# Kernel tuning notes

Hardware: AMD Instinct MI355X
Metric: run time of the kernel (lower is better)

Reference implementation:

```python
import jax, jax.numpy as jnp
import numpy as np

B, T, D = 2, 2048, 1024
H = 16
HD = D // H  # 64
A = 16
MLP_H = 4 * D
EPS = 1e-6


def rmsnorm(x, w):
    # x: [..., C], w: [C]
    return x * jax.lax.rsqrt(jnp.mean(x * x, axis=-1, keepdims=True) + EPS) * w


def setup_inputs() -> dict:
    key = jax.random.key(0)
    ks = jax.random.split(key, 24)
    s = 0.02
    inp = {
        'x': jax.random.normal(ks[0], (B, T, D), jnp.float32),
        'actions': jax.random.normal(ks[1], (B, T, A), jnp.float32),
        # block norms
        'n1_w': jnp.ones((D,), jnp.float32),
        'n2_w': jnp.ones((D,), jnp.float32),
        # attention projections (stored [in, out])
        'q_w': jax.random.normal(ks[2], (D, D), jnp.float32) * s,
        'q_b': jnp.zeros((D,), jnp.float32),
        'k_w': jax.random.normal(ks[3], (D, D), jnp.float32) * s,
        'k_b': jnp.zeros((D,), jnp.float32),
        'v_w': jax.random.normal(ks[4], (D, D), jnp.float32) * s,
        'v_b': jnp.zeros((D,), jnp.float32),
        'qn_w': jnp.ones((HD,), jnp.float32),
        'kn_w': jnp.ones((HD,), jnp.float32),
        'o_w': jax.random.normal(ks[5], (D, D), jnp.float32) * s,
        'o_b': jnp.zeros((D,), jnp.float32),
        # action conditioning
        'ae1_w': jax.random.normal(ks[6], (A, D), jnp.float32) * s,
        'ae1_b': jnp.zeros((D,), jnp.float32),
        'ae2_w': jax.random.normal(ks[7], (D, D), jnp.float32) * s,
        'ae2_b': jnp.zeros((D,), jnp.float32),
        'mod_w': jax.random.normal(ks[8], (D, 4 * D), jnp.float32) * s,
        'mod_b': jnp.zeros((4 * D,), jnp.float32),
        # mlp
        'm1_w': jax.random.normal(ks[9], (D, MLP_H), jnp.float32) * s,
        'm1_b': jnp.zeros((MLP_H,), jnp.float32),
        'm2_w': jax.random.normal(ks[10], (MLP_H, D), jnp.float32) * s,
        'm2_b': jnp.zeros((D,), jnp.float32),
    }
    return inp


def _forward(x, actions, n1_w, n2_w, q_w, q_b, k_w, k_b, v_w, v_b, qn_w, kn_w,
             o_w, o_b, ae1_w, ae1_b, ae2_w, ae2_b, mod_w, mod_b,
             m1_w, m1_b, m2_w, m2_b):
    Bc, Tc, Dc = x.shape
    scale = HD ** -0.5

    # --- causal temporal attention with QK RMSNorm ---
    h = rmsnorm(x, n1_w)
    q = (h @ q_w + q_b).reshape(Bc, Tc, H, HD).transpose(0, 2, 1, 3)  # [B,H,T,hd]
    k = (h @ k_w + k_b).reshape(Bc, Tc, H, HD).transpose(0, 2, 1, 3)
    v = (h @ v_w + v_b).reshape(Bc, Tc, H, HD).transpose(0, 2, 1, 3)
    q = rmsnorm(q, qn_w)
    k = rmsnorm(k, kn_w)
    attn = jnp.einsum('bhqd,bhkd->bhqk', q, k) * scale
    causal = jnp.triu(jnp.ones((Tc, Tc), bool), k=1)  # True above diagonal -> masked
    attn = jnp.where(causal, -jnp.inf, attn)
    attn = jax.nn.softmax(attn, axis=-1)
    out = jnp.einsum('bhqk,bhkd->bhqd', attn, v)
    out = out.transpose(0, 2, 1, 3).reshape(Bc, Tc, Dc)
    x = x + (out @ o_w + o_b)

    # --- action conditioning (AdaLN-style; eval mode, no dropout) ---
    ae = jax.nn.silu(actions @ ae1_w + ae1_b) @ ae2_w + ae2_b  # [B,T,D]
    mod = jax.nn.silu(ae) @ mod_w + mod_b  # [B,T,4D]
    shift1, scale1, _, _ = jnp.split(mod, 4, axis=-1)
    x = x * (1.0 + scale1) + shift1

    # --- MLP ---
    h2 = rmsnorm(x, n2_w)
    x = x + (jax.nn.gelu(h2 @ m1_w + m1_b, approximate=False) @ m2_w + m2_b)
    return x


def reference(x, actions, n1_w, n2_w, q_w, q_b, k_w, k_b, v_w, v_b, qn_w, kn_w,
              o_w, o_b, ae1_w, ae1_b, ae2_w, ae2_b, mod_w, mod_b,
              m1_w, m1_b, m2_w, m2_b):
    return _forward(x, actions, n1_w, n2_w, q_w, q_b, k_w, k_b, v_w, v_b,
                    qn_w, kn_w, o_w, o_b, ae1_w, ae1_b, ae2_w, ae2_b,
                    mod_w, mod_b, m1_w, m1_b, m2_w, m2_b)
```

## Files before the change

kernel.cpp:

```cpp
#include <hip/hip_runtime.h>
#include <hip/hip_bf16.h>
#include <math.h>

typedef __hip_bfloat16 bf16;
typedef __attribute__((ext_vector_type(8))) short short8;
typedef __attribute__((ext_vector_type(4))) float float4_;

#define B_   2
#define T_   2048
#define D_   1024
#define H_   16
#define NTOK (B_ * T_)
#define QSCALE 0.18033688011112042f

#define AS1 __attribute__((address_space(1)))
#define AS3 __attribute__((address_space(3)))

static __device__ __forceinline__ float b2f(bf16 v) { return __bfloat162float(v); }
static __device__ __forceinline__ bf16  f2b(float v) { return __float2bfloat16(v); }
static __device__ __forceinline__ short f2s(float v) {
    unsigned u = __builtin_bit_cast(unsigned, v);
    unsigned r = (u + 0x7FFFu + ((u >> 16) & 1u)) >> 16;
    return (short)r;
}
static __device__ __forceinline__ float to_f(float v) { return v; }
static __device__ __forceinline__ float to_f(bf16 v) { return __bfloat162float(v); }
static __device__ __forceinline__ void  store_o(float* p, float v) { *p = v; }
static __device__ __forceinline__ void  store_o(bf16* p, float v) { *p = __float2bfloat16(v); }
static __device__ __forceinline__ void gl_lds16(const void* g, void* l) {
    __builtin_amdgcn_global_load_lds((const AS1 unsigned int*)g, (AS3 unsigned int*)l, 16, 0, 0);
}

__global__ __launch_bounds__(256) void rmsnorm_k(const float* __restrict__ x,
                                                 const float* __restrict__ w,
                                                 bf16* __restrict__ out) {
    int t = blockIdx.x, tid = threadIdx.x;
    float xs[4], ss = 0.f;
#pragma unroll
    for (int i = 0; i < 4; ++i) {
        float v = x[(size_t)t * D_ + tid + i * 256];
        xs[i] = v; ss += v * v;
    }
    __shared__ float red[4];
#pragma unroll
    for (int off = 32; off > 0; off >>= 1) ss += __shfl_xor(ss, off, 64);
    if ((tid & 63) == 0) red[tid >> 6] = ss;
    __syncthreads();
    ss = red[0] + red[1] + red[2] + red[3];
    float inv = rsqrtf(ss * (1.f / D_) + 1e-6f);
#pragma unroll
    for (int i = 0; i < 4; ++i) {
        int c = tid + i * 256;
        out[(size_t)t * D_ + c] = f2b(xs[i] * inv * w[c]);
    }
}

__global__ __launch_bounds__(256) void modnorm_k(float* __restrict__ x1,
                                                 const bf16* __restrict__ mod,
                                                 const float* __restrict__ w,
                                                 bf16* __restrict__ h2) {
    int t = blockIdx.x, tid = threadIdx.x;
    float xs[4], ss = 0.f;
#pragma unroll
    for (int i = 0; i < 4; ++i) {
        int c = tid + i * 256;
        float sh = b2f(mod[(size_t)t * 2048 + c]);
        float sc = b2f(mod[(size_t)t * 2048 + 1024 + c]);
        float v = x1[(size_t)t * D_ + c] * (1.f + sc) + sh;
        xs[i] = v; ss += v * v;
        x1[(size_t)t * D_ + c] = v;
    }
    __shared__ float red[4];
#pragma unroll
    for (int off = 32; off > 0; off >>= 1) ss += __shfl_xor(ss, off, 64);
    if ((tid & 63) == 0) red[tid >> 6] = ss;
    __syncthreads();
    ss = red[0] + red[1] + red[2] + red[3];
    float inv = rsqrtf(ss * (1.f / D_) + 1e-6f);
#pragma unroll
    for (int i = 0; i < 4; ++i) {
        int c = tid + i * 256;
        h2[(size_t)t * D_ + c] = f2b(xs[i] * inv * w[c]);
    }
}

__global__ __launch_bounds__(256) void ae1_k(const float* __restrict__ actions,
                                             const float* __restrict__ w,
                                             const float* __restrict__ b,
                                             bf16* __restrict__ out) {
    int t = blockIdx.x, tid = threadIdx.x;
    float av[16];
#pragma unroll
    for (int a = 0; a < 16; ++a) av[a] = actions[(size_t)t * 16 + a];
#pragma unroll
    for (int i = 0; i < 4; ++i) {
        int n = tid + i * 256;
        float acc = b[n];
#pragma unroll
        for (int a = 0; a < 16; ++a) acc += av[a] * w[a * D_ + n];
        out[(size_t)t * D_ + n] = f2b(acc / (1.f + expf(-acc)));
    }
}

struct WD { const float* src; bf16* dst; int K, N, ldw, tiles; };
struct WPack { WD d[8]; };
__global__ __launch_bounds__(256) void wprep_k(WPack p) {
    int bid = blockIdx.x;
    int mi = 0, cum = 0;
#pragma unroll
    for (mi = 0; mi < 8; ++mi) {
        if (bid < cum + p.d[mi].tiles) break;
        cum += p.d[mi].tiles;
    }
    if (mi >= 8) return;
    WD w = p.d[mi];
    int local = bid - cum;
    int tilesK = w.K >> 6;
    int tk = local % tilesK, tn = local / tilesK;
    int k0 = tk * 64, n0 = tn * 64;
    __shared__ short Tt[64 * 72];
    int t = threadIdx.x;
    int row = t >> 2, seg = t & 3;
    const float* sp = w.src + (size_t)(k0 + row) * w.ldw + n0 + seg * 16;
#pragma unroll
    for (int q = 0; q < 4; ++q) {
        float4_ f = *(const float4_*)(sp + q * 4);
#pragma unroll
        for (int j = 0; j < 4; ++j) Tt[(seg * 16 + q * 4 + j) * 72 + row] = f2s(f[j]);
    }
    __syncthreads();
    bf16* dp = w.dst + (size_t)(n0 + row) * w.K + k0 + seg * 16;
    *(short8*)dp       = *(const short8*)&Tt[row * 72 + seg * 16];
    *(short8*)(dp + 8) = *(const short8*)&Tt[row * 72 + seg * 16 + 8];
}

__global__ __launch_bounds__(256) void bcat_k(const float* __restrict__ qb,
                                              const float* __restrict__ kb,
                                              const float* __restrict__ vb,
                                              float* __restrict__ dst) {
    int i = blockIdx.x * 256 + threadIdx.x;
    const float* s = (i < 1024) ? qb : (i < 2048) ? kb : vb;
    dst[i] = s[i & 1023];
}

template <int ACT, int QKN, typename ResT, typename OutT>
__global__ __launch_bounds__(256) void gemm_k(const bf16* __restrict__ A,
                                              const bf16* __restrict__ Bt,
                                              const float* __restrict__ bias,
                                              const ResT* __restrict__ res,
                                              OutT* __restrict__ out,
                                              int M, int N, int K, int ldo,
                                              const float* __restrict__ qn_w,
                                              const float* __restrict__ kn_w) {
    __shared__ __align__(16) short As[128 * 64];
    __shared__ __align__(16) short Bs[128 * 64];
    const int tid = threadIdx.x;
    const int bm = blockIdx.y * 128, bn = blockIdx.x * 128;
    const int wave = tid >> 6, lane = tid & 63;
    const int wm = (wave & 1) * 64, wn = (wave >> 1) * 64;
    const int l15 = lane & 15, quad = lane >> 4;
    const int lrow = lane >> 3, lseg = (lane & 7) * 8;
    float4_ acc[4][4] = {};

    for (int k0 = 0; k0 < K; k0 += 64) {
#pragma unroll
        for (int it = 0; it < 4; ++it) {
            int r = it * 32 + wave * 8;
            gl_lds16((const short*)A + (size_t)(bm + r + lrow) * K + k0 + lseg, &As[r * 64]);
            gl_lds16((const short*)Bt + (size_t)(bn + r + lrow) * K + k0 + lseg, &Bs[r * 64]);
        }
        __syncthreads();
#pragma unroll
        for (int kk = 0; kk < 64; kk += 32) {
            short8 af[4], bfr[4];
#pragma unroll
            for (int i = 0; i < 4; ++i)
                af[i] = *(const short8*)&As[(wm + i * 16 + l15) * 64 + kk + quad * 8];
#pragma unroll
            for (int j = 0; j < 4; ++j)
                bfr[j] = *(const short8*)&Bs[(wn + j * 16 + l15) * 64 + kk + quad * 8];
#pragma unroll
            for (int i = 0; i < 4; ++i)
#pragma unroll
                for (int j = 0; j < 4; ++j)
                    acc[i][j] = __builtin_amdgcn_mfma_f32_16x16x32_bf16(af[i], bfr[j], acc[i][j], 0, 0, 0);
        }
        __syncthreads();
    }

    int seg = (bn + wn) >> 10;
    float nwv[4];
    if (QKN && seg < 2) {
        const float* nw = seg ? kn_w : qn_w;
        float qsc = seg ? 1.f : QSCALE;
#pragma unroll
        for (int j = 0; j < 4; ++j) nwv[j] = nw[j * 16 + l15] * qsc;
    }

#pragma unroll
    for (int i = 0; i < 4; ++i) {
        float vv[4][4];
#pragma unroll
        for (int j = 0; j < 4; ++j) {
            float bv = bias[bn + wn + j * 16 + l15];
#pragma unroll
            for (int r = 0; r < 4; ++r) vv[j][r] = acc[i][j][r] + bv;
        }
        if (QKN && seg < 2) {
#pragma unroll
            for (int r = 0; r < 4; ++r) {
                float ss = vv[0][r] * vv[0][r] + vv[1][r] * vv[1][r]
                         + vv[2][r] * vv[2][r] + vv[3][r] * vv[3][r];
#pragma unroll
                for (int off = 8; off > 0; off >>= 1) ss += __shfl_xor(ss, off, 16);
                float inv = rsqrtf(ss * (1.f / 64.f) + 1e-6f);
#pragma unroll
                for (int j = 0; j < 4; ++j) vv[j][r] *= inv * nwv[j];
            }
        }
#pragma unroll
        for (int j = 0; j < 4; ++j) {
            int col = bn + wn + j * 16 + l15;
#pragma unroll
            for (int r = 0; r < 4; ++r) {
                int row = bm + wm + i * 16 + quad * 4 + r;
                float v = vv[j][r];
                if (ACT == 1) v = v / (1.f + expf(-v));
                else if (ACT == 2) v = 0.5f * v * (1.f + erff(v * 0.70710678118654752f));
                if (res) v += to_f(res[(size_t)row * ldo + col]);
                store_o(&out[(size_t)row * ldo + col], v);
            }
        }
    }
}

template <int ACT, typename ResT, typename OutT>
__global__ __launch_bounds__(256) void gemm64_k(const bf16* __restrict__ A,
                                                const bf16* __restrict__ Bt,
                                                const float* __restrict__ bias,
                                                const ResT* __restrict__ res,
                                                OutT* __restrict__ out,
                                                int M, int N, int K) {
    __shared__ __align__(16) short As[64 * 64];
    __shared__ __align__(16) short Bs[128 * 64];
    const int tid = threadIdx.x;
    const int bm = blockIdx.y * 64, bn = blockIdx.x * 128;
    const int wave = tid >> 6, lane = tid & 63;
    const int wm = (wave & 1) * 32, wn = (wave >> 1) * 64;
    const int l15 = lane & 15, quad = lane >> 4;
    const int lrow = lane >> 3, lseg = (lane & 7) * 8;
    float4_ acc[2][4] = {};

    for (int k0 = 0; k0 < K; k0 += 64) {
#pragma unroll
        for (int it = 0; it < 2; ++it) {
            int r = wave * 16 + it * 8;
            gl_lds16((const short*)A + (size_t)(bm + r + lrow) * K + k0 + lseg, &As[r * 64]);
        }
#pragma unroll
        for (int it = 0; it < 4; ++it) {
            int r = it * 32 + wave * 8;
            gl_lds16((const short*)Bt + (size_t)(bn + r + lrow) * K + k0 + lseg, &Bs[r * 64]);
        }
        __syncthreads();
#pragma unroll
        for (int kk = 0; kk < 64; kk += 32) {
            short8 af[2], bfr[4];
#pragma unroll
            for (int i = 0; i < 2; ++i)
                af[i] = *(const short8*)&As[(wm + i * 16 + l15) * 64 + kk + quad * 8];
#pragma unroll
            for (int j = 0; j < 4; ++j)
                bfr[j] = *(const short8*)&Bs[(wn + j * 16 + l15) * 64 + kk + quad * 8];
#pragma unroll
            for (int i = 0; i < 2; ++i)
#pragma unroll
                for (int j = 0; j < 4; ++j)
                    acc[i][j] = __builtin_amdgcn_mfma_f32_16x16x32_bf16(af[i], bfr[j], acc[i][j], 0, 0, 0);
        }
        __syncthreads();
    }

#pragma unroll
    for (int i = 0; i < 2; ++i)
#pragma unroll
        for (int j = 0; j < 4; ++j) {
            int col = bn + wn + j * 16 + l15;
            float bv = bias[col];
#pragma unroll
            for (int r = 0; r < 4; ++r) {
                int row = bm + wm + i * 16 + quad * 4 + r;
                float v = acc[i][j][r] + bv;
                if (ACT == 1) v = v / (1.f + expf(-v));
                else if (ACT == 2) v = 0.5f * v * (1.f + erff(v * 0.70710678118654752f));
                if (res) v += to_f(res[(size_t)row * N + col]);
                store_o(&out[(size_t)row * N + col], v);
            }
        }
}

static __device__ __forceinline__ int chunk_base(int qb) {
    return (qb < 16) ? (qb - 8) * 2
         : (qb < 24) ? 16 + (qb - 16) * 3
                     : 40 + (qb - 24) * 4;
}

template <int SPLIT>
__global__ __launch_bounds__(256) void attn_k(const bf16* __restrict__ QKV,
                                              bf16* __restrict__ O,
                                              float* __restrict__ OP,
                                              float* __restrict__ LP) {
    __shared__ __align__(16) short Vt[2][64 * 72];
    __shared__ __align__(16) short Ps[4][16 * 72];
    const int bh = blockIdx.y, b = bh >> 4, h = bh & 15;
    int qb, ci;
    if (SPLIT) {
        int idx = 79 - (int)blockIdx.x;
        if (idx < 8)       { qb = idx; ci = 0; }
        else if (idx < 24) { qb = 8 + ((idx - 8) >> 1); ci = (idx - 8) & 1; }
        else if (idx < 48) { int u = idx - 24; int q3 = u / 3; qb = 16 + q3; ci = u - q3 * 3; }
        else               { int u = idx - 48; qb = 24 + (u >> 2); ci = u & 3; }
    } else { qb = 31 - (int)blockIdx.x; ci = 0; }
    const int n   = qb + 1;
    const int nc  = SPLIT ? ((qb >> 3) + 1) : 1;
    const int bsz = n / nc, rem = n - bsz * nc;
    const int t0  = ci * bsz + (ci < rem ? ci : rem);
    const int t1  = t0 + bsz + (ci < rem ? 1 : 0);
    const int q0  = qb * 64;
    const int tid = threadIdx.x, wave = tid >> 6, lane = tid & 63;
    const int l15 = lane & 15, quad = lane >> 4;
    const size_t base = (size_t)b * T_ * 3072 + h * 64;
    const short* Qp = (const short*)QKV + base;
    const short* Kp = Qp + 1024;
    const short* Vp = Qp + 2048;

    const int qrow = q0 + wave * 16 + l15;
    short8 qf0 = *(const short8*)(Qp + (size_t)qrow * 3072 + quad * 8);
    short8 qf1 = *(const short8*)(Qp + (size_t)qrow * 3072 + 32 + quad * 8);

    float4_ oacc[4] = {};
    float l_r[4] = {0.f, 0.f, 0.f, 0.f};

    const int vrow = tid >> 2, vseg = tid & 3;

    {
        const short* vp = Vp + (size_t)(t0 * 64 + vrow) * 3072 + vseg * 16;
        short8 v0 = *(const short8*)vp;
        short8 v1 = *(const short8*)(vp + 8);
#pragma unroll
        for (int j = 0; j < 8; ++j) Vt[0][(vseg * 16 + j) * 72 + vrow] = v0[j];
#pragma unroll
        for (int j = 0; j < 8; ++j) Vt[0][(vseg * 16 + 8 + j) * 72 + vrow] = v1[j];
    }
    __syncthreads();

    for (int t = t0; t < t1; ++t) {
        const int kv0 = t * 64, buf = (t - t0) & 1;
        if (t + 1 < t1) {
            const short* vp = Vp + (size_t)((t + 1) * 64 + vrow) * 3072 + vseg * 16;
            short8 v0 = *(const short8*)vp;
            short8 v1 = *(const short8*)(vp + 8);
#pragma unroll
            for (int j = 0; j < 8; ++j) Vt[buf ^ 1][(vseg * 16 + j) * 72 + vrow] = v0[j];
#pragma unroll
            for (int j = 0; j < 8; ++j) Vt[buf ^ 1][(vseg * 16 + 8 + j) * 72 + vrow] = v1[j];
        }

        float4_ s[4];
#pragma unroll
        for (int c = 0; c < 4; ++c) {
            const short* kp = Kp + (size_t)(kv0 + c * 16 + l15) * 3072 + quad * 8;
            short8 kb0 = *(const short8*)kp;
            short8 kb1 = *(const short8*)(kp + 32);
            float4_ sc = {};
            sc = __builtin_amdgcn_mfma_f32_16x16x32_bf16(qf0, kb0, sc, 0, 0, 0);
            sc = __builtin_amdgcn_mfma_f32_16x16x32_bf16(qf1, kb1, sc, 0, 0, 0);
            s[c] = sc;
        }

        if (t == qb) {
#pragma unroll
            for (int r = 0; r < 4; ++r) {
                int qr = q0 + wave * 16 + quad * 4 + r;
#pragma unroll
                for (int c = 0; c < 4; ++c) {
                    int kvi = kv0 + c * 16 + l15;
                    float p = __builtin_amdgcn_exp2f(s[c][r]);
                    p = (kvi > qr) ? 0.f : p;
                    s[c][r] = p;
                    l_r[r] += p;
                }
            }
        } else {
#pragma unroll
            for (int r = 0; r < 4; ++r)
#pragma unroll
                for (int c = 0; c < 4; ++c) {
                    float p = __builtin_amdgcn_exp2f(s[c][r]);
                    s[c][r] = p;
                    l_r[r] += p;
                }
        }

#pragma unroll
        for (int c = 0; c < 4; ++c) {
            int pk01, pk23;
            asm("v_cvt_pk_bf16_f32 %0, %1, %2" : "=v"(pk01) : "v"(s[c][0]), "v"(s[c][1]));
            asm("v_cvt_pk_bf16_f32 %0, %1, %2" : "=v"(pk23) : "v"(s[c][2]), "v"(s[c][3]));
            short* pp = &Ps[wave][(quad * 4) * 72 + c * 16 + l15];
            pp[0]   = (short)pk01;
            pp[72]  = (short)(((unsigned)pk01) >> 16);
            pp[144] = (short)pk23;
            pp[216] = (short)(((unsigned)pk23) >> 16);
        }

#pragma unroll
        for (int kk = 0; kk < 64; kk += 32) {
            short8 pf = *(const short8*)&Ps[wave][l15 * 72 + kk + quad * 8];
#pragma unroll
            for (int d = 0; d < 4; ++d) {
                short8 vf = *(const short8*)&Vt[buf][(d * 16 + l15) * 72 + kk + quad * 8];
                oacc[d] = __builtin_amdgcn_mfma_f32_16x16x32_bf16(pf, vf, oacc[d], 0, 0, 0);
            }
        }
        __syncthreads();
    }

    float lsum[4];
#pragma unroll
    for (int r = 0; r < 4; ++r) {
        float l = l_r[r];
#pragma unroll
        for (int off = 8; off > 0; off >>= 1) l += __shfl_xor(l, off, 16);
        lsum[r] = l;
    }

    if (!SPLIT || nc == 1) {
#pragma unroll
        for (int d = 0; d < 4; ++d)
#pragma unroll
            for (int r = 0; r < 4; ++r) {
                int qr = q0 + wave * 16 + quad * 4 + r;
                O[(size_t)(b * T_ + qr) * D_ + h * 64 + d * 16 + l15] = f2b(oacc[d][r] / lsum[r]);
            }
    } else {
        const int slot = bh * 72 + chunk_base(qb) + ci;
        float* op = OP + (size_t)slot * 4096;
#pragma unroll
        for (int d = 0; d < 4; ++d)
#pragma unroll
            for (int r = 0; r < 4; ++r)
                op[(wave * 16 + quad * 4 + r) * 64 + d * 16 + l15] = oacc[d][r];
        if (l15 == 0) {
#pragma unroll
            for (int r = 0; r < 4; ++r)
                LP[slot * 64 + wave * 16 + quad * 4 + r] = lsum[r];
        }
    }
}

__global__ __launch_bounds__(256) void comb_k(const float* __restrict__ OP,
                                              const float* __restrict__ LP,
                                              bf16* __restrict__ O) {
    const int qb = 8 + (int)blockIdx.x;
    const int bh = blockIdx.y, b = bh >> 4, h = bh & 15;
    const int nc = (qb >> 3) + 1;
    const int slot0 = bh * 72 + chunk_base(qb);
    const int tid = threadIdx.x;
    const int row = tid >> 2, c0 = (tid & 3) << 4;
    const float* p = OP + (size_t)slot0 * 4096 + row * 64 + c0;
    float4_ a0 = *(const float4_*)(p + 0);
    float4_ a1 = *(const float4_*)(p + 4);
    float4_ a2 = *(const float4_*)(p + 8);
    float4_ a3 = *(const float4_*)(p + 12);
    float l = LP[slot0 * 64 + row];
    for (int c = 1; c < nc; ++c) {
        const float* q = p + (size_t)c * 4096;
        a0 += *(const float4_*)(q + 0);
        a1 += *(const float4_*)(q + 4);
        a2 += *(const float4_*)(q + 8);
        a3 += *(const float4_*)(q + 12);
        l += LP[(slot0 + c) * 64 + row];
    }
    float inv = 1.f / l;
    short8 w0, w1;
#pragma unroll
    for (int j = 0; j < 4; ++j) {
        w0[j]     = f2s(a0[j] * inv);
        w0[4 + j] = f2s(a1[j] * inv);
        w1[j]     = f2s(a2[j] * inv);
        w1[4 + j] = f2s(a3[j] * inv);
    }
    bf16* o = O + (size_t)(b * T_ + qb * 64 + row) * D_ + h * 64 + c0;
    *(short8*)o       = w0;
    *(short8*)(o + 8) = w1;
}

extern "C" void kernel_launch(void* const* d_in, const int* in_sizes, int n_in,
                              void* d_out, int out_size, void* d_ws, size_t ws_size,
                              hipStream_t stream) {
    const float* x     = (const float*)d_in[0];
    const float* acts  = (const float*)d_in[1];
    const float* n1_w  = (const float*)d_in[2];
    const float* n2_w  = (const float*)d_in[3];
    const float* q_w   = (const float*)d_in[4];
    const float* q_b   = (const float*)d_in[5];
    const float* k_w   = (const float*)d_in[6];
    const float* k_b   = (const float*)d_in[7];
    const float* v_w   = (const float*)d_in[8];
    const float* v_b   = (const float*)d_in[9];
    const float* qn_w  = (const float*)d_in[10];
    const float* kn_w  = (const float*)d_in[11];
    const float* o_w   = (const float*)d_in[12];
    const float* o_b   = (const float*)d_in[13];
    const float* ae1_w = (const float*)d_in[14];
    const float* ae1_b = (const float*)d_in[15];
    const float* ae2_w = (const float*)d_in[16];
    const float* ae2_b = (const float*)d_in[17];
    const float* mod_w = (const float*)d_in[18];
    const float* mod_b = (const float*)d_in[19];
    const float* m1_w  = (const float*)d_in[20];
    const float* m1_b  = (const float*)d_in[21];
    const float* m2_w  = (const float*)d_in[22];
    const float* m2_b  = (const float*)d_in[23];
    float* out = (float*)d_out;

    char* ws = (char*)d_ws;
    const size_t MB = 1ull << 20;
    bf16*  Ah   = (bf16*)(ws + 0);
    bf16*  QKVp = (bf16*)(ws + 8 * MB);
    bf16*  AO   = (bf16*)(ws + 32 * MB);
    bf16*  AE1  = (bf16*)(ws + 8 * MB);
    bf16*  AES  = (bf16*)(ws + 16 * MB);
    bf16*  MOD  = (bf16*)(ws + 24 * MB);
    bf16*  M1G  = (bf16*)(ws + 8 * MB);
    float* X1   = out;

    bf16* WTqkv = (bf16*)(ws + 40 * MB);
    bf16* WTo   = (bf16*)(ws + 46 * MB);
    bf16* WTae2 = (bf16*)(ws + 48 * MB);
    bf16* WTmod = (bf16*)(ws + 50 * MB);
    bf16* WTm1  = (bf16*)(ws + 54 * MB);
    bf16* WTm2  = (bf16*)(ws + 62 * MB);
    float* biasQKV = (float*)(ws + 70 * MB);
    float* OPART = (float*)(ws + 70 * MB + 16384);
    float* LPART = (float*)(ws + 70 * MB + 16384 + 37748736);
    const bool split = ws_size >= (70 * MB + 16384 + 37748736ull + 589824ull);

    dim3 blk(256);

    WPack p;
    p.d[0] = { q_w,   WTqkv,                1024, 1024, 1024, 256 };
    p.d[1] = { k_w,   WTqkv + 1024 * 1024,  1024, 1024, 1024, 256 };
    p.d[2] = { v_w,   WTqkv + 2048 * 1024,  1024, 1024, 1024, 256 };
    p.d[3] = { o_w,   WTo,   1024, 1024, 1024, 256 };
    p.d[4] = { ae2_w, WTae2, 1024, 1024, 1024, 256 };
    p.d[5] = { mod_w, WTmod, 1024, 2048, 4096, 512 };
    p.d[6] = { m1_w,  WTm1,  1024, 4096, 4096, 1024 };
    p.d[7] = { m2_w,  WTm2,  4096, 1024, 1024, 1024 };
    wprep_k<<<3840, blk, 0, stream>>>(p);
    bcat_k<<<12, blk, 0, stream>>>(q_b, k_b, v_b, biasQKV);

    rmsnorm_k<<<NTOK, blk, 0, stream>>>(x, n1_w, Ah);
    gemm_k<0, 1, float, bf16><<<dim3(24, 32), blk, 0, stream>>>(Ah, WTqkv, biasQKV, (const float*)nullptr, QKVp, NTOK, 3072, 1024, 3072, qn_w, kn_w);
    if (split) {
        attn_k<1><<<dim3(80, B_ * H_), blk, 0, stream>>>(QKVp, AO, OPART, LPART);
        comb_k<<<dim3(24, B_ * H_), blk, 0, stream>>>(OPART, LPART, AO);
    } else {
        attn_k<0><<<dim3(32, B_ * H_), blk, 0, stream>>>(QKVp, AO, OPART, LPART);
    }
    gemm64_k<0, float, float><<<dim3(8, 64), blk, 0, stream>>>(AO, WTo, o_b, x, X1, NTOK, 1024, 1024);
    ae1_k<<<NTOK, blk, 0, stream>>>(acts, ae1_w, ae1_b, AE1);
    gemm64_k<1, float, bf16><<<dim3(8, 64), blk, 0, stream>>>(AE1, WTae2, ae2_b, (const float*)nullptr, AES, NTOK, 1024, 1024);
    gemm_k<0, 0, float, bf16><<<dim3(16, 32), blk, 0, stream>>>(AES, WTmod, mod_b, (const float*)nullptr, MOD, NTOK, 2048, 1024, 2048, nullptr, nullptr);
    modnorm_k<<<NTOK, blk, 0, stream>>>(X1, MOD, n2_w, Ah);
    gemm_k<2, 0, float, bf16><<<dim3(32, 32), blk, 0, stream>>>(Ah, WTm1, m1_b, (const float*)nullptr, M1G, NTOK, 4096, 1024, 4096, nullptr, nullptr);
    gemm64_k<0, float, float><<<dim3(8, 64), blk, 0, stream>>>(M1G, WTm2, m2_b, X1, out, NTOK, 1024, 4096);
}
```

Before: 558.8 us.

## Emit V pre-transposed from a separate GEMM and drop LDS staging in attention

V is now computed by its own GEMM with swapped operands and a per-row bias, so it lands in a head-major transposed layout, while Q/K come from a narrower 2048-wide GEMM. The attention kernel drops its shared-memory V transpose and P staging: scores are computed transposed, P is rearranged into MFMA operand form with cross-lane shuffles, and V fragments are read straight from global memory. This removes the syncthreads and LDS traffic and lets more blocks run per CU. It also adds a finer KV split (CSH=2, 144 blocks per head) when the workspace is large enough. The extra GEMM launch and uncached global V loads could offset part of the savings.

```diff
diff --git a/kernel.cpp b/kernel.cpp
--- a/kernel.cpp
+++ b/kernel.cpp
@@ -5,6 +5,7 @@
 typedef __hip_bfloat16 bf16;
 typedef __attribute__((ext_vector_type(8))) short short8;
 typedef __attribute__((ext_vector_type(4))) float float4_;
+typedef __attribute__((ext_vector_type(4))) int int4_;
 
 #define B_   2
 #define T_   2048
@@ -136,14 +137,12 @@
 
 __global__ __launch_bounds__(256) void bcat_k(const float* __restrict__ qb,
                                               const float* __restrict__ kb,
-                                              const float* __restrict__ vb,
                                               float* __restrict__ dst) {
     int i = blockIdx.x * 256 + threadIdx.x;
-    const float* s = (i < 1024) ? qb : (i < 2048) ? kb : vb;
-    dst[i] = s[i & 1023];
-}
-
-template <int ACT, int QKN, typename ResT, typename OutT>
+    dst[i] = (i < 1024) ? qb[i] : kb[i & 1023];
+}
+
+template <int ACT, int QKN, int BROW, typename ResT, typename OutT>
 __global__ __launch_bounds__(256) void gemm_k(const bf16* __restrict__ A,
                                               const bf16* __restrict__ Bt,
                                               const float* __restrict__ bias,
@@ -200,11 +199,16 @@
 #pragma unroll
     for (int i = 0; i < 4; ++i) {
         float vv[4][4];
+        float bvr[4];
+        if (BROW) {
+#pragma unroll
+            for (int r = 0; r < 4; ++r) bvr[r] = bias[bm + wm + i * 16 + quad * 4 + r];
+        }
 #pragma unroll
         for (int j = 0; j < 4; ++j) {
-            float bv = bias[bn + wn + j * 16 + l15];
-#pragma unroll
-            for (int r = 0; r < 4; ++r) vv[j][r] = acc[i][j][r] + bv;
+            float bv = BROW ? 0.f : bias[bn + wn + j * 16 + l15];
+#pragma unroll
+            for (int r = 0; r < 4; ++r) vv[j][r] = acc[i][j][r] + (BROW ? bvr[r] : bv);
         }
         if (QKN && seg < 2) {
 #pragma unroll
@@ -299,173 +303,145 @@
         }
 }
 
-static __device__ __forceinline__ int chunk_base(int qb) {
-    return (qb < 16) ? (qb - 8) * 2
-         : (qb < 24) ? 16 + (qb - 16) * 3
-                     : 40 + (qb - 24) * 4;
-}
-
-template <int SPLIT>
-__global__ __launch_bounds__(256) void attn_k(const bf16* __restrict__ QKV,
-                                              bf16* __restrict__ O,
-                                              float* __restrict__ OP,
-                                              float* __restrict__ LP) {
-    __shared__ __align__(16) short Vt[2][64 * 72];
-    __shared__ __align__(16) short Ps[4][16 * 72];
+template <int CSH>
+static __device__ __forceinline__ int chunk_base2(int qb) {
+    int g = qb >> CSH, S = 1 << CSH;
+    return (g == 0) ? 0 : S * ((g - 1) * (g + 2) / 2) + (qb & (S - 1)) * (g + 1);
+}
+
+template <int SPLIT, int CSH>
+__global__ __launch_bounds__(256, 4) void attn_k(const bf16* __restrict__ QK,
+                                                 const bf16* __restrict__ VT,
+                                                 bf16* __restrict__ O,
+                                                 float* __restrict__ OP,
+                                                 float* __restrict__ LP) {
     const int bh = blockIdx.y, b = bh >> 4, h = bh & 15;
     int qb, ci;
     if (SPLIT) {
-        int idx = 79 - (int)blockIdx.x;
-        if (idx < 8)       { qb = idx; ci = 0; }
-        else if (idx < 24) { qb = 8 + ((idx - 8) >> 1); ci = (idx - 8) & 1; }
-        else if (idx < 48) { int u = idx - 24; int q3 = u / 3; qb = 16 + q3; ci = u - q3 * 3; }
-        else               { int u = idx - 48; qb = 24 + (u >> 2); ci = u & 3; }
+        int rem = blockIdx.x; qb = 31; ci = 0;
+        for (;;) { int ncq = (qb >> CSH) + 1; if (rem < ncq) { ci = rem; break; } rem -= ncq; --qb; }
     } else { qb = 31 - (int)blockIdx.x; ci = 0; }
     const int n   = qb + 1;
-    const int nc  = SPLIT ? ((qb >> 3) + 1) : 1;
-    const int bsz = n / nc, rem = n - bsz * nc;
-    const int t0  = ci * bsz + (ci < rem ? ci : rem);
-    const int t1  = t0 + bsz + (ci < rem ? 1 : 0);
+    const int nc  = SPLIT ? ((qb >> CSH) + 1) : 1;
+    const int bsz = n / nc, rem2 = n - bsz * nc;
+    const int t0  = ci * bsz + (ci < rem2 ? ci : rem2);
+    const int t1  = t0 + bsz + (ci < rem2 ? 1 : 0);
     const int q0  = qb * 64;
     const int tid = threadIdx.x, wave = tid >> 6, lane = tid & 63;
     const int l15 = lane & 15, quad = lane >> 4;
-    const size_t base = (size_t)b * T_ * 3072 + h * 64;
-    const short* Qp = (const short*)QKV + base;
+
+    const short* Qp = (const short*)QK + (size_t)b * T_ * 2048 + h * 64;
     const short* Kp = Qp + 1024;
-    const short* Vp = Qp + 2048;
+    const short* Vp = (const short*)VT + (size_t)h * 64 * 4096 + b * T_;
 
     const int qrow = q0 + wave * 16 + l15;
-    short8 qf0 = *(const short8*)(Qp + (size_t)qrow * 3072 + quad * 8);
-    short8 qf1 = *(const short8*)(Qp + (size_t)qrow * 3072 + 32 + quad * 8);
+    short8 qf0 = *(const short8*)(Qp + (size_t)qrow * 2048 + quad * 8);
+    short8 qf1 = *(const short8*)(Qp + (size_t)qrow * 2048 + 32 + quad * 8);
 
     float4_ oacc[4] = {};
-    float l_r[4] = {0.f, 0.f, 0.f, 0.f};
-
-    const int vrow = tid >> 2, vseg = tid & 3;
-
-    {
-        const short* vp = Vp + (size_t)(t0 * 64 + vrow) * 3072 + vseg * 16;
-        short8 v0 = *(const short8*)vp;
-        short8 v1 = *(const short8*)(vp + 8);
-#pragma unroll
-        for (int j = 0; j < 8; ++j) Vt[0][(vseg * 16 + j) * 72 + vrow] = v0[j];
-#pragma unroll
-        for (int j = 0; j < 8; ++j) Vt[0][(vseg * 16 + 8 + j) * 72 + vrow] = v1[j];
-    }
-    __syncthreads();
+    float l_r = 0.f;
 
     for (int t = t0; t < t1; ++t) {
-        const int kv0 = t * 64, buf = (t - t0) & 1;
-        if (t + 1 < t1) {
-            const short* vp = Vp + (size_t)((t + 1) * 64 + vrow) * 3072 + vseg * 16;
-            short8 v0 = *(const short8*)vp;
-            short8 v1 = *(const short8*)(vp + 8);
-#pragma unroll
-            for (int j = 0; j < 8; ++j) Vt[buf ^ 1][(vseg * 16 + j) * 72 + vrow] = v0[j];
-#pragma unroll
-            for (int j = 0; j < 8; ++j) Vt[buf ^ 1][(vseg * 16 + 8 + j) * 72 + vrow] = v1[j];
-        }
-
+        const int kv0 = t * 64;
         float4_ s[4];
 #pragma unroll
         for (int c = 0; c < 4; ++c) {
-            const short* kp = Kp + (size_t)(kv0 + c * 16 + l15) * 3072 + quad * 8;
+            const short* kp = Kp + (size_t)(kv0 + c * 16 + l15) * 2048 + quad * 8;
             short8 kb0 = *(const short8*)kp;
             short8 kb1 = *(const short8*)(kp + 32);
             float4_ sc = {};
-            sc = __builtin_amdgcn_mfma_f32_16x16x32_bf16(qf0, kb0, sc, 0, 0, 0);
-            sc = __builtin_amdgcn_mfma_f32_16x16x32_bf16(qf1, kb1, sc, 0, 0, 0);
+            sc = __builtin_amdgcn_mfma_f32_16x16x32_bf16(kb0, qf0, sc, 0, 0, 0);
+            sc = __builtin_amdgcn_mfma_f32_16x16x32_bf16(kb1, qf1, sc, 0, 0, 0);
             s[c] = sc;
         }
-
         if (t == qb) {
+#pragma unroll
+            for (int c = 0; c < 4; ++c)
+#pragma unroll
+                for (int r = 0; r < 4; ++r) {
+                    int kvi = kv0 + c * 16 + quad * 4 + r;
+                    float p = __builtin_amdgcn_exp2f(s[c][r]);
+                    p = (kvi > qrow) ? 0.f : p;
+                    s[c][r] = p; l_r += p;
+                }
+        } else {
+#pragma unroll
+            for (int c = 0; c < 4; ++c)
+#pragma unroll
+                for (int r = 0; r < 4; ++r) {
+                    float p = __builtin_amdgcn_exp2f(s[c][r]);
+                    s[c][r] = p; l_r += p;
+                }
+        }
+        int pk0[4], pk1[4];
+#pragma unroll
+        for (int c = 0; c < 4; ++c) {
+            asm("v_cvt_pk_bf16_f32 %0, %1, %2" : "=v"(pk0[c]) : "v"(s[c][0]), "v"(s[c][1]));
+            asm("v_cvt_pk_bf16_f32 %0, %1, %2" : "=v"(pk1[c]) : "v"(s[c][2]), "v"(s[c][3]));
+        }
+        short8 pa[2];
+#pragma unroll
+        for (int x = 0; x < 2; ++x) {
+            int own0 = (quad & 2) ? pk0[2 * x + 1] : pk0[2 * x];
+            int own1 = (quad & 2) ? pk1[2 * x + 1] : pk1[2 * x];
+            int oth0 = (quad & 2) ? pk0[2 * x]     : pk0[2 * x + 1];
+            int oth1 = (quad & 2) ? pk1[2 * x]     : pk1[2 * x + 1];
+            int a16_0 = __shfl_xor(own0, 16, 64), a16_1 = __shfl_xor(own1, 16, 64);
+            int a32_0 = __shfl_xor(oth0, 32, 64), a32_1 = __shfl_xor(oth1, 32, 64);
+            int a48_0 = __shfl_xor(oth0, 48, 64), a48_1 = __shfl_xor(oth1, 48, 64);
+            int u0 = (quad == 0) ? own0  : (quad == 1) ? a48_0 : (quad == 2) ? a32_0 : a16_0;
+            int u1 = (quad == 0) ? own1  : (quad == 1) ? a48_1 : (quad == 2) ? a32_1 : a16_1;
+            int u2 = (quad == 0) ? a16_0 : (quad == 1) ? a32_0 : (quad == 2) ? a48_0 : own0;
+            int u3 = (quad == 0) ? a16_1 : (quad == 1) ? a32_1 : (quad == 2) ? a48_1 : own1;
+            int4_ pi = { u0, u1, u2, u3 };
+            pa[x] = __builtin_bit_cast(short8, pi);
+        }
+#pragma unroll
+        for (int x = 0; x < 2; ++x)
+#pragma unroll
+            for (int d = 0; d < 4; ++d) {
+                short8 vf = *(const short8*)(Vp + (size_t)(d * 16 + l15) * 4096 + kv0 + x * 32 + quad * 8);
+                oacc[d] = __builtin_amdgcn_mfma_f32_16x16x32_bf16(pa[x], vf, oacc[d], 0, 0, 0);
+            }
+    }
+
+    l_r += __shfl_xor(l_r, 16, 64);
+    l_r += __shfl_xor(l_r, 32, 64);
+
+    if (!SPLIT || nc == 1) {
+        float linv = 1.f / l_r;
+        float lrow[4];
+#pragma unroll
+        for (int r = 0; r < 4; ++r) lrow[r] = __shfl(linv, quad * 4 + r, 64);
+#pragma unroll
+        for (int d = 0; d < 4; ++d)
 #pragma unroll
             for (int r = 0; r < 4; ++r) {
                 int qr = q0 + wave * 16 + quad * 4 + r;
-#pragma unroll
-                for (int c = 0; c < 4; ++c) {
-                    int kvi = kv0 + c * 16 + l15;
-                    float p = __builtin_amdgcn_exp2f(s[c][r]);
-                    p = (kvi > qr) ? 0.f : p;
-                    s[c][r] = p;
-                    l_r[r] += p;
-                }
-            }
-        } else {
-#pragma unroll
-            for (int r = 0; r < 4; ++r)
-#pragma unroll
-                for (int c = 0; c < 4; ++c) {
-                    float p = __builtin_amdgcn_exp2f(s[c][r]);
-                    s[c][r] = p;
-                    l_r[r] += p;
-                }
-        }
-
-#pragma unroll
-        for (int c = 0; c < 4; ++c) {
-            int pk01, pk23;
-            asm("v_cvt_pk_bf16_f32 %0, %1, %2" : "=v"(pk01) : "v"(s[c][0]), "v"(s[c][1]));
-            asm("v_cvt_pk_bf16_f32 %0, %1, %2" : "=v"(pk23) : "v"(s[c][2]), "v"(s[c][3]));
-            short* pp = &Ps[wave][(quad * 4) * 72 + c * 16 + l15];
-            pp[0]   = (short)pk01;
-            pp[72]  = (short)(((unsigned)pk01) >> 16);
-            pp[144] = (short)pk23;
-            pp[216] = (short)(((unsigned)pk23) >> 16);
-        }
-
-#pragma unroll
-        for (int kk = 0; kk < 64; kk += 32) {
-            short8 pf = *(const short8*)&Ps[wave][l15 * 72 + kk + quad * 8];
-#pragma unroll
-            for (int d = 0; d < 4; ++d) {
-                short8 vf = *(const short8*)&Vt[buf][(d * 16 + l15) * 72 + kk + quad * 8];
-                oacc[d] = __builtin_amdgcn_mfma_f32_16x16x32_bf16(pf, vf, oacc[d], 0, 0, 0);
-            }
-        }
-        __syncthreads();
-    }
-
-    float lsum[4];
-#pragma unroll
-    for (int r = 0; r < 4; ++r) {
-        float l = l_r[r];
-#pragma unroll
-        for (int off = 8; off > 0; off >>= 1) l += __shfl_xor(l, off, 16);
-        lsum[r] = l;
-    }
-
-    if (!SPLIT || nc == 1) {
-#pragma unroll
-        for (int d = 0; d < 4; ++d)
-#pragma unroll
-            for (int r = 0; r < 4; ++r) {
-                int qr = q0 + wave * 16 + quad * 4 + r;
-                O[(size_t)(b * T_ + qr) * D_ + h * 64 + d * 16 + l15] = f2b(oacc[d][r] / lsum[r]);
+                O[(size_t)(b * T_ + qr) * D_ + h * 64 + d * 16 + l15] = f2b(oacc[d][r] * lrow[r]);
             }
     } else {
-        const int slot = bh * 72 + chunk_base(qb) + ci;
+        const int SLOTS = chunk_base2<CSH>(32);
+        const int slot = bh * SLOTS + chunk_base2<CSH>(qb) + ci;
         float* op = OP + (size_t)slot * 4096;
 #pragma unroll
         for (int d = 0; d < 4; ++d)
 #pragma unroll
             for (int r = 0; r < 4; ++r)
                 op[(wave * 16 + quad * 4 + r) * 64 + d * 16 + l15] = oacc[d][r];
-        if (l15 == 0) {
-#pragma unroll
-            for (int r = 0; r < 4; ++r)
-                LP[slot * 64 + wave * 16 + quad * 4 + r] = lsum[r];
-        }
-    }
-}
-
+        if (lane < 16) LP[slot * 64 + wave * 16 + lane] = l_r;
+    }
+}
+
+template <int CSH>
 __global__ __launch_bounds__(256) void comb_k(const float* __restrict__ OP,
                                               const float* __restrict__ LP,
                                               bf16* __restrict__ O) {
-    const int qb = 8 + (int)blockIdx.x;
+    const int qb = (1 << CSH) + (int)blockIdx.x;
     const int bh = blockIdx.y, b = bh >> 4, h = bh & 15;
-    const int nc = (qb >> 3) + 1;
-    const int slot0 = bh * 72 + chunk_base(qb);
+    const int nc = (qb >> CSH) + 1;
+    const int SLOTS = chunk_base2<CSH>(32);
+    const int slot0 = bh * SLOTS + chunk_base2<CSH>(qb);
     const int tid = threadIdx.x;
     const int row = tid >> 2, c0 = (tid & 3) << 4;
     const float* p = OP + (size_t)slot0 * 4096 + row * 64 + c0;
@@ -528,7 +504,8 @@
     char* ws = (char*)d_ws;
     const size_t MB = 1ull << 20;
     bf16*  Ah   = (bf16*)(ws + 0);
-    bf16*  QKVp = (bf16*)(ws + 8 * MB);
+    bf16*  QKp  = (bf16*)(ws + 8 * MB);
+    bf16*  VT4  = (bf16*)(ws + 24 * MB);
     bf16*  AO   = (bf16*)(ws + 32 * MB);
     bf16*  AE1  = (bf16*)(ws + 8 * MB);
     bf16*  AES  = (bf16*)(ws + 16 * MB);
@@ -537,15 +514,19 @@
     float* X1   = out;
 
     bf16* WTqkv = (bf16*)(ws + 40 * MB);
+    bf16* WTv   = WTqkv + 2048 * 1024;
     bf16* WTo   = (bf16*)(ws + 46 * MB);
     bf16* WTae2 = (bf16*)(ws + 48 * MB);
     bf16* WTmod = (bf16*)(ws + 50 * MB);
     bf16* WTm1  = (bf16*)(ws + 54 * MB);
     bf16* WTm2  = (bf16*)(ws + 62 * MB);
-    float* biasQKV = (float*)(ws + 70 * MB);
-    float* OPART = (float*)(ws + 70 * MB + 16384);
-    float* LPART = (float*)(ws + 70 * MB + 16384 + 37748736);
-    const bool split = ws_size >= (70 * MB + 16384 + 37748736ull + 589824ull);
+    float* biasQK = (float*)(ws + 70 * MB);
+    float* OPART  = (float*)(ws + 70 * MB + 16384);
+    const size_t base_ws = 70 * MB + 16384;
+    const size_t need2 = base_ws + 73400320ull + 32 * 140 * 256ull;
+    const size_t need3 = base_ws + 37748736ull + 32 * 72 * 256ull;
+    const int mode = (ws_size >= need2) ? 2 : (ws_size >= need3) ? 3 : 0;
+    float* LPART = (float*)(ws + base_ws + (mode == 2 ? 73400320ull : 37748736ull));
 
     dim3 blk(256);
 
@@ -559,21 +540,25 @@
     p.d[6] = { m1_w,  WTm1,  1024, 4096, 4096, 1024 };
     p.d[7] = { m2_w,  WTm2,  4096, 1024, 1024, 1024 };
     wprep_k<<<3840, blk, 0, stream>>>(p);
-    bcat_k<<<12, blk, 0, stream>>>(q_b, k_b, v_b, biasQKV);
+    bcat_k<<<8, blk, 0, stream>>>(q_b, k_b, biasQK);
 
     rmsnorm_k<<<NTOK, blk, 0, stream>>>(x, n1_w, Ah);
-    gemm_k<0, 1, float, bf16><<<dim3(24, 32), blk, 0, stream>>>(Ah, WTqkv, biasQKV, (const float*)nullptr, QKVp, NTOK, 3072, 1024, 3072, qn_w, kn_w);
-    if (split) {
-        attn_k<1><<<dim3(80, B_ * H_), blk, 0, stream>>>(QKVp, AO, OPART, LPART);
-        comb_k<<<dim3(24, B_ * H_), blk, 0, stream>>>(OPART, LPART, AO);
+    gemm_k<0, 1, 0, float, bf16><<<dim3(16, 32), blk, 0, stream>>>(Ah, WTqkv, biasQK, (const float*)nullptr, QKp, NTOK, 2048, 1024, 2048, qn_w, kn_w);
+    gemm_k<0, 0, 1, float, bf16><<<dim3(32, 8), blk, 0, stream>>>(WTv, Ah, v_b, (const float*)nullptr, VT4, 1024, 4096, 1024, 4096, nullptr, nullptr);
+    if (mode == 2) {
+        attn_k<1, 2><<<dim3(144, B_ * H_), blk, 0, stream>>>(QKp, VT4, AO, OPART, LPART);
+        comb_k<2><<<dim3(28, B_ * H_), blk, 0, stream>>>(OPART, LPART, AO);
+    } else if (mode == 3) {
+        attn_k<1, 3><<<dim3(80, B_ * H_), blk, 0, stream>>>(QKp, VT4, AO, OPART, LPART);
+        comb_k<3><<<dim3(24, B_ * H_), blk, 0, stream>>>(OPART, LPART, AO);
     } else {
-        attn_k<0><<<dim3(32, B_ * H_), blk, 0, stream>>>(QKVp, AO, OPART, LPART);
+        attn_k<0, 3><<<dim3(32, B_ * H_), blk, 0, stream>>>(QKp, VT4, AO, OPART, LPART);
     }
     gemm64_k<0, float, float><<<dim3(8, 64), blk, 0, stream>>>(AO, WTo, o_b, x, X1, NTOK, 1024, 1024);
     ae1_k<<<NTOK, blk, 0, stream>>>(acts, ae1_w, ae1_b, AE1);
     gemm64_k<1, float, bf16><<<dim3(8, 64), blk, 0, stream>>>(AE1, WTae2, ae2_b, (const float*)nullptr, AES, NTOK, 1024, 1024);
-    gemm_k<0, 0, float, bf16><<<dim3(16, 32), blk, 0, stream>>>(AES, WTmod, mod_b, (const float*)nullptr, MOD, NTOK, 2048, 1024, 2048, nullptr, nullptr);
+    gemm_k<0, 0, 0, float, bf16><<<dim3(16, 32), blk, 0, stream>>>(AES, WTmod, mod_b, (const float*)nullptr, MOD, NTOK, 2048, 1024, 2048, nullptr, nullptr);
     modnorm_k<<<NTOK, blk, 0, stream>>>(X1, MOD, n2_w, Ah);
-    gemm_k<2, 0, float, bf16><<<dim3(32, 32), blk, 0, stream>>>(Ah, WTm1, m1_b, (const float*)nullptr, M1G, NTOK, 4096, 1024, 4096, nullptr, nullptr);
+    gemm_k<2, 0, 0, float, bf16><<<dim3(32, 32), blk, 0, stream>>>(Ah, WTm1, m1_b, (const float*)nullptr, M1G, NTOK, 4096, 1024, 4096, nullptr, nullptr);
     gemm64_k<0, float, float><<<dim3(8, 64), blk, 0, stream>>>(M1G, WTm2, m2_b, X1, out, NTOK, 1024, 4096);
 }
```

Result: slower. 619.4 us (+10.8%).

## Produce V transposed from a separate GEMM and stream it to LDS in attention

Applied to the files above, without the earlier changes.

The fused QKV projection is split into a QK GEMM and a separate V GEMM that computes V^T (weights times activations) with a per-row bias, writing V in a [head_dim, token] layout. The attention kernel then loads V tiles directly into a swizzled LDS buffer with global-to-LDS copies instead of transposing them element by element through shared memory. The goal is to remove the scalar LDS transpose stores and the bank conflicts in the attention inner loop. The cost is one extra GEMM launch, and the transposed GEMM has a different grid shape.

```diff
diff --git a/kernel.cpp b/kernel.cpp
--- a/kernel.cpp
+++ b/kernel.cpp
@@ -136,14 +136,12 @@
 
 __global__ __launch_bounds__(256) void bcat_k(const float* __restrict__ qb,
                                               const float* __restrict__ kb,
-                                              const float* __restrict__ vb,
                                               float* __restrict__ dst) {
     int i = blockIdx.x * 256 + threadIdx.x;
-    const float* s = (i < 1024) ? qb : (i < 2048) ? kb : vb;
-    dst[i] = s[i & 1023];
-}
-
-template <int ACT, int QKN, typename ResT, typename OutT>
+    dst[i] = (i < 1024) ? qb[i] : kb[i & 1023];
+}
+
+template <int ACT, int QKN, int BROW, typename ResT, typename OutT>
 __global__ __launch_bounds__(256) void gemm_k(const bf16* __restrict__ A,
                                               const bf16* __restrict__ Bt,
                                               const float* __restrict__ bias,
@@ -200,11 +198,16 @@
 #pragma unroll
     for (int i = 0; i < 4; ++i) {
         float vv[4][4];
+        float bvr[4];
+        if (BROW) {
+#pragma unroll
+            for (int r = 0; r < 4; ++r) bvr[r] = bias[bm + wm + i * 16 + quad * 4 + r];
+        }
 #pragma unroll
         for (int j = 0; j < 4; ++j) {
-            float bv = bias[bn + wn + j * 16 + l15];
-#pragma unroll
-            for (int r = 0; r < 4; ++r) vv[j][r] = acc[i][j][r] + bv;
+            float bv = BROW ? 0.f : bias[bn + wn + j * 16 + l15];
+#pragma unroll
+            for (int r = 0; r < 4; ++r) vv[j][r] = acc[i][j][r] + (BROW ? bvr[r] : bv);
         }
         if (QKN && seg < 2) {
 #pragma unroll
@@ -306,11 +309,12 @@
 }
 
 template <int SPLIT>
-__global__ __launch_bounds__(256) void attn_k(const bf16* __restrict__ QKV,
+__global__ __launch_bounds__(256) void attn_k(const bf16* __restrict__ QK,
+                                              const bf16* __restrict__ VT,
                                               bf16* __restrict__ O,
                                               float* __restrict__ OP,
                                               float* __restrict__ LP) {
-    __shared__ __align__(16) short Vt[2][64 * 72];
+    __shared__ __align__(16) short Vs[2][64 * 64];
     __shared__ __align__(16) short Ps[4][16 * 72];
     const int bh = blockIdx.y, b = bh >> 4, h = bh & 15;
     int qb, ci;
@@ -329,47 +333,44 @@
     const int q0  = qb * 64;
     const int tid = threadIdx.x, wave = tid >> 6, lane = tid & 63;
     const int l15 = lane & 15, quad = lane >> 4;
-    const size_t base = (size_t)b * T_ * 3072 + h * 64;
-    const short* Qp = (const short*)QKV + base;
-    const short* Kp = Qp + 1024;
-    const short* Vp = Qp + 2048;
+
+    const short* Qp  = (const short*)QK + (size_t)b * T_ * 2048 + h * 64;
+    const short* Kp  = Qp + 1024;
+    const short* Vtp = (const short*)VT + (size_t)h * 64 * 4096 + b * T_;
 
     const int qrow = q0 + wave * 16 + l15;
-    short8 qf0 = *(const short8*)(Qp + (size_t)qrow * 3072 + quad * 8);
-    short8 qf1 = *(const short8*)(Qp + (size_t)qrow * 3072 + 32 + quad * 8);
+    short8 qf0 = *(const short8*)(Qp + (size_t)qrow * 2048 + quad * 8);
+    short8 qf1 = *(const short8*)(Qp + (size_t)qrow * 2048 + 32 + quad * 8);
 
     float4_ oacc[4] = {};
     float l_r[4] = {0.f, 0.f, 0.f, 0.f};
 
-    const int vrow = tid >> 2, vseg = tid & 3;
+    const int slr  = lane >> 3;
+    const int sblk = (lane & 7) ^ slr;
 
     {
-        const short* vp = Vp + (size_t)(t0 * 64 + vrow) * 3072 + vseg * 16;
-        short8 v0 = *(const short8*)vp;
-        short8 v1 = *(const short8*)(vp + 8);
-#pragma unroll
-        for (int j = 0; j < 8; ++j) Vt[0][(vseg * 16 + j) * 72 + vrow] = v0[j];
-#pragma unroll
-        for (int j = 0; j < 8; ++j) Vt[0][(vseg * 16 + 8 + j) * 72 + vrow] = v1[j];
+#pragma unroll
+        for (int it = 0; it < 2; ++it) {
+            int r = it * 32 + wave * 8;
+            gl_lds16(Vtp + (size_t)(r + slr) * 4096 + t0 * 64 + sblk * 8, &Vs[0][r * 64]);
+        }
     }
     __syncthreads();
 
     for (int t = t0; t < t1; ++t) {
         const int kv0 = t * 64, buf = (t - t0) & 1;
         if (t + 1 < t1) {
-            const short* vp = Vp + (size_t)((t + 1) * 64 + vrow) * 3072 + vseg * 16;
-            short8 v0 = *(const short8*)vp;
-            short8 v1 = *(const short8*)(vp + 8);
-#pragma unroll
-            for (int j = 0; j < 8; ++j) Vt[buf ^ 1][(vseg * 16 + j) * 72 + vrow] = v0[j];
-#pragma unroll
-            for (int j = 0; j < 8; ++j) Vt[buf ^ 1][(vseg * 16 + 8 + j) * 72 + vrow] = v1[j];
+#pragma unroll
+            for (int it = 0; it < 2; ++it) {
+                int r = it * 32 + wave * 8;
+                gl_lds16(Vtp + (size_t)(r + slr) * 4096 + kv0 + 64 + sblk * 8, &Vs[buf ^ 1][r * 64]);
+            }
         }
 
         float4_ s[4];
 #pragma unroll
         for (int c = 0; c < 4; ++c) {
-            const short* kp = Kp + (size_t)(kv0 + c * 16 + l15) * 3072 + quad * 8;
+            const short* kp = Kp + (size_t)(kv0 + c * 16 + l15) * 2048 + quad * 8;
             short8 kb0 = *(const short8*)kp;
             short8 kb1 = *(const short8*)(kp + 32);
             float4_ sc = {};
@@ -414,12 +415,13 @@
             pp[216] = (short)(((unsigned)pk23) >> 16);
         }
 
+        const int vkey = (l15 & 7) * 8;
 #pragma unroll
         for (int kk = 0; kk < 64; kk += 32) {
             short8 pf = *(const short8*)&Ps[wave][l15 * 72 + kk + quad * 8];
 #pragma unroll
             for (int d = 0; d < 4; ++d) {
-                short8 vf = *(const short8*)&Vt[buf][(d * 16 + l15) * 72 + kk + quad * 8];
+                short8 vf = *(const short8*)&Vs[buf][(d * 16 + l15) * 64 + ((kk + quad * 8) ^ vkey)];
                 oacc[d] = __builtin_amdgcn_mfma_f32_16x16x32_bf16(pf, vf, oacc[d], 0, 0, 0);
             }
         }
@@ -528,7 +530,8 @@
     char* ws = (char*)d_ws;
     const size_t MB = 1ull << 20;
     bf16*  Ah   = (bf16*)(ws + 0);
-    bf16*  QKVp = (bf16*)(ws + 8 * MB);
+    bf16*  QKp  = (bf16*)(ws + 8 * MB);
+    bf16*  VT4  = (bf16*)(ws + 24 * MB);
     bf16*  AO   = (bf16*)(ws + 32 * MB);
     bf16*  AE1  = (bf16*)(ws + 8 * MB);
     bf16*  AES  = (bf16*)(ws + 16 * MB);
@@ -537,14 +540,15 @@
     float* X1   = out;
 
     bf16* WTqkv = (bf16*)(ws + 40 * MB);
+    bf16* WTv   = WTqkv + 2048 * 1024;
     bf16* WTo   = (bf16*)(ws + 46 * MB);
     bf16* WTae2 = (bf16*)(ws + 48 * MB);
     bf16* WTmod = (bf16*)(ws + 50 * MB);
     bf16* WTm1  = (bf16*)(ws + 54 * MB);
     bf16* WTm2  = (bf16*)(ws + 62 * MB);
-    float* biasQKV = (float*)(ws + 70 * MB);
-    float* OPART = (float*)(ws + 70 * MB + 16384);
-    float* LPART = (float*)(ws + 70 * MB + 16384 + 37748736);
+    float* biasQK = (float*)(ws + 70 * MB);
+    float* OPART  = (float*)(ws + 70 * MB + 16384);
+    float* LPART  = (float*)(ws + 70 * MB + 16384 + 37748736);
     const bool split = ws_size >= (70 * MB + 16384 + 37748736ull + 589824ull);
 
     dim3 blk(256);
@@ -559,21 +563,22 @@
     p.d[6] = { m1_w,  WTm1,  1024, 4096, 4096, 1024 };
     p.d[7] = { m2_w,  WTm2,  4096, 1024, 1024, 1024 };
     wprep_k<<<3840, blk, 0, stream>>>(p);
-    bcat_k<<<12, blk, 0, stream>>>(q_b, k_b, v_b, biasQKV);
+    bcat_k<<<8, blk, 0, stream>>>(q_b, k_b, biasQK);
 
     rmsnorm_k<<<NTOK, blk, 0, stream>>>(x, n1_w, Ah);
-    gemm_k<0, 1, float, bf16><<<dim3(24, 32), blk, 0, stream>>>(Ah, WTqkv, biasQKV, (const float*)nullptr, QKVp, NTOK, 3072, 1024, 3072, qn_w, kn_w);
+    gemm_k<0, 1, 0, float, bf16><<<dim3(16, 32), blk, 0, stream>>>(Ah, WTqkv, biasQK, (const float*)nullptr, QKp, NTOK, 2048, 1024, 2048, qn_w, kn_w);
+    gemm_k<0, 0, 1, float, bf16><<<dim3(32, 8), blk, 0, stream>>>(WTv, Ah, v_b, (const float*)nullptr, VT4, 1024, 4096, 1024, 4096, nullptr, nullptr);
     if (split) {
-        attn_k<1><<<dim3(80, B_ * H_), blk, 0, stream>>>(QKVp, AO, OPART, LPART);
+        attn_k<1><<<dim3(80, B_ * H_), blk, 0, stream>>>(QKp, VT4, AO, OPART, LPART);
         comb_k<<<dim3(24, B_ * H_), blk, 0, stream>>>(OPART, LPART, AO);
     } else {
-        attn_k<0><<<dim3(32, B_ * H_), blk, 0, stream>>>(QKVp, AO, OPART, LPART);
+        attn_k<0><<<dim3(32, B_ * H_), blk, 0, stream>>>(QKp, VT4, AO, OPART, LPART);
     }
     gemm64_k<0, float, float><<<dim3(8, 64), blk, 0, stream>>>(AO, WTo, o_b, x, X1, NTOK, 1024, 1024);
     ae1_k<<<NTOK, blk, 0, stream>>>(acts, ae1_w, ae1_b, AE1);
     gemm64_k<1, float, bf16><<<dim3(8, 64), blk, 0, stream>>>(AE1, WTae2, ae2_b, (const float*)nullptr, AES, NTOK, 1024, 1024);
-    gemm_k<0, 0, float, bf16><<<dim3(16, 32), blk, 0, stream>>>(AES, WTmod, mod_b, (const float*)nullptr, MOD, NTOK, 2048, 1024, 2048, nullptr, nullptr);
+    gemm_k<0, 0, 0, float, bf16><<<dim3(16, 32), blk, 0, stream>>>(AES, WTmod, mod_b, (const float*)nullptr, MOD, NTOK, 2048, 1024, 2048, nullptr, nullptr);
     modnorm_k<<<NTOK, blk, 0, stream>>>(X1, MOD, n2_w, Ah);
-    gemm_k<2, 0, float, bf16><<<dim3(32, 32), blk, 0, stream>>>(Ah, WTm1, m1_b, (const float*)nullptr, M1G, NTOK, 4096, 1024, 4096, nullptr, nullptr);
+    gemm_k<2, 0, 0, float, bf16><<<dim3(32, 32), blk, 0, stream>>>(Ah, WTm1, m1_b, (const float*)nullptr, M1G, NTOK, 4096, 1024, 4096, nullptr, nullptr);
     gemm64_k<0, float, float><<<dim3(8, 64), blk, 0, stream>>>(M1G, WTm2, m2_b, X1, out, NTOK, 1024, 4096);
 }
```

New measurement: 564.4 us. Within noise of the previous version (+1.0%).
